# Kernel optimization log

Hardware: AMD Instinct MI355X
Metric: run time of the kernel (lower is better)

## Reference

```python
import jax, jax.numpy as jnp
import numpy as np

N_NODES = 100000
N_EDGES = 1000000
EMB = 64
HID = 64
N_CLASSES = 1
LEAKY_SLOPE = 0.01  # flax.linen.leaky_relu default


def setup_inputs() -> dict:
    key = jax.random.key(0)
    k1, k2, k3, k4, k5 = jax.random.split(key, 5)
    node_ids = jnp.arange(N_NODES, dtype=jnp.int32)
    senders = jax.random.randint(k1, (N_EDGES,), 0, N_NODES, dtype=jnp.int32)
    receivers = jax.random.randint(k2, (N_EDGES,), 0, N_NODES, dtype=jnp.int32)
    embed_table = jax.random.normal(k3, (N_NODES, EMB), dtype=jnp.float32) * 0.05
    W1 = jax.random.normal(k4, (EMB, HID), dtype=jnp.float32) * (1.0 / np.sqrt(EMB))
    W2 = jax.random.normal(k5, (HID, N_CLASSES), dtype=jnp.float32) * (1.0 / np.sqrt(HID))
    b2 = jnp.zeros((N_CLASSES,), dtype=jnp.float32)
    return {"node_ids": node_ids, "senders": senders, "receivers": receivers,
            "embed_table": embed_table, "W1": W1, "W2": W2, "b2": b2}


def gcn_aggregate(x, senders, receivers, n_nodes, symmetric):
    # Faithful to jraph.GraphConvolution: update_node_fn is applied BEFORE this.
    if symmetric:
        ones = jnp.ones_like(senders, dtype=x.dtype)
        send_deg = jax.ops.segment_sum(ones, senders, num_segments=n_nodes)
        recv_deg = jax.ops.segment_sum(ones, receivers, num_segments=n_nodes)
        x = x * jax.lax.rsqrt(jnp.maximum(send_deg, 1.0))[:, None]
        x = jax.ops.segment_sum(x[senders], receivers, num_segments=n_nodes)  # [N, d]
        x = x * jax.lax.rsqrt(jnp.maximum(recv_deg, 1.0))[:, None]
    else:
        x = jax.ops.segment_sum(x[senders], receivers, num_segments=n_nodes)
    return x


def reference(node_ids, senders, receivers, embed_table, W1, W2, b2):
    n = node_ids.shape[0]
    # GraphMapFeatures(embed_node_fn=nn.Embed(...))
    x = embed_table[node_ids]                      # [N, EMB]
    # GraphConvolution(Dense(hidden, use_bias=False), symmetric_normalization=True)
    x = x @ W1                                     # [N, HID]
    x = gcn_aggregate(x, senders, receivers, n, symmetric=True)
    x = jax.nn.leaky_relu(x, negative_slope=LEAKY_SLOPE)
    # GraphConvolution(Dense(classes), symmetric_normalization=False)
    x = x @ W2 + b2                                # [N, C]
    x = gcn_aggregate(x, senders, receivers, n, symmetric=False)
    return jax.nn.sigmoid(x)
```

## Files before the change

kernel.cpp:

```cpp
#include <hip/hip_runtime.h>
#include <hip/hip_bf16.h>

#define N_NODES 100000
#define N_EDGES 1000000
#define SCAN_B 256
#define N_BLOCKS_SCAN ((N_NODES + SCAN_B - 1) / SCAN_B)
#define H_BLOCKS 1024

#define CHUNKS 40
#define CHUNK_E 25000
#define HWORDS 25000


__device__ __forceinline__ unsigned f32_to_bf16(float v) {
    unsigned u = __float_as_uint(v);
    return (u + 0x7fffu + ((u >> 16) & 1u)) >> 16;
}

__global__ void k_hist8(const int4* __restrict__ s4,
                        const int4* __restrict__ r4,
                        unsigned* __restrict__ ghist_s8,
                        unsigned* __restrict__ ghist_r8,
                        unsigned char* __restrict__ rank8) {
    __shared__ unsigned lds[HWORDS];
    int b   = blockIdx.x;
    int isR = (b < CHUNKS);
    int c   = isR ? b : b - CHUNKS;
    int t   = threadIdx.x;

    for (int w = t; w < HWORDS; w += 1024) lds[w] = 0u;
    __syncthreads();

    int beg = c * (CHUNK_E / 4);
    int end = beg + CHUNK_E / 4;
    if (isR) {
        for (int q = beg + t; q < end; q += 1024) {
            int4 v = r4[q];
            int sh0 = (v.x & 3) * 8, sh1 = (v.y & 3) * 8;
            int sh2 = (v.z & 3) * 8, sh3 = (v.w & 3) * 8;
            unsigned o0 = atomicAdd(&lds[v.x >> 2], 1u << sh0);
            unsigned o1 = atomicAdd(&lds[v.y >> 2], 1u << sh1);
            unsigned o2 = atomicAdd(&lds[v.z >> 2], 1u << sh2);
            unsigned o3 = atomicAdd(&lds[v.w >> 2], 1u << sh3);
            uchar4 rk;
            rk.x = (unsigned char)((o0 >> sh0) & 0xffu);
            rk.y = (unsigned char)((o1 >> sh1) & 0xffu);
            rk.z = (unsigned char)((o2 >> sh2) & 0xffu);
            rk.w = (unsigned char)((o3 >> sh3) & 0xffu);
            *(uchar4*)(rank8 + 4 * (size_t)q) = rk;
        }
    } else {
        for (int q = beg + t; q < end; q += 1024) {
            int4 v = s4[q];
            atomicAdd(&lds[v.x >> 2], 1u << ((v.x & 3) * 8));
            atomicAdd(&lds[v.y >> 2], 1u << ((v.y & 3) * 8));
            atomicAdd(&lds[v.z >> 2], 1u << ((v.z & 3) * 8));
            atomicAdd(&lds[v.w >> 2], 1u << ((v.w & 3) * 8));
        }
    }
    __syncthreads();

    uint4* __restrict__ dst =
        (uint4*)((isR ? ghist_r8 : ghist_s8) + (size_t)c * HWORDS);
    const uint4* lsrc = (const uint4*)lds;
    for (int w = t; w < HWORDS / 4; w += 1024) dst[w] = lsrc[w];
}

__global__ void k_scanA(const unsigned char* __restrict__ gs8,
                        const unsigned char* __restrict__ gr8,
                        unsigned char* __restrict__ base8,
                        int* __restrict__ cnt_r,
                        float* __restrict__ rs,
                        int* __restrict__ blockSums) {
    __shared__ int s[SCAN_B];
    int t = threadIdx.x;
    int idx = blockIdx.x * SCAN_B + t;
    int v = 0;
    if (idx < N_NODES) {
        unsigned ss = 0;
#pragma unroll
        for (int c = 0; c < CHUNKS; ++c) ss += gs8[(size_t)c * N_NODES + idx];
        rs[idx] = rsqrtf(fmaxf((float)ss, 1.0f));
        unsigned run = 0;
#pragma unroll
        for (int c = 0; c < CHUNKS; ++c) {
            base8[(size_t)c * N_NODES + idx] = (unsigned char)run;
            run += gr8[(size_t)c * N_NODES + idx];
        }
        v = (int)run;
        cnt_r[idx] = v;
    }
    s[t] = v;
    __syncthreads();
    for (int off = 1; off < SCAN_B; off <<= 1) {
        int x = (t >= off) ? s[t - off] : 0;
        __syncthreads();
        s[t] += x;
        __syncthreads();
    }
    if (t == SCAN_B - 1) blockSums[blockIdx.x] = s[t];
}

__global__ void k_scanCD_h(const int* __restrict__ cnt_r,
                           const int* __restrict__ blockSums,
                           int* __restrict__ row_start,
                           const float* __restrict__ emb,
                           const float* __restrict__ rs,
                           const float* __restrict__ W1,
                           unsigned short* __restrict__ h16) {
    __shared__ int s[SCAN_B];
    int t = threadIdx.x;
    int b = blockIdx.x;

    if (b < N_BLOCKS_SCAN) {
        int acc = 0;
        for (int j = t; j < b; j += SCAN_B) acc += blockSums[j];
        s[t] = acc;
        __syncthreads();
        for (int off = SCAN_B / 2; off > 0; off >>= 1) {
            if (t < off) s[t] += s[t + off];
            __syncthreads();
        }
        int blockOff = s[0];
        __syncthreads();

        int idx = b * SCAN_B + t;
        int v = (idx < N_NODES) ? cnt_r[idx] : 0;
        s[t] = v;
        __syncthreads();
        for (int off = 1; off < SCAN_B; off <<= 1) {
            int x = (t >= off) ? s[t - off] : 0;
            __syncthreads();
            s[t] += x;
            __syncthreads();
        }
        if (idx < N_NODES) row_start[idx] = blockOff + s[t] - v;
        if (b == 0 && t == 0) row_start[N_NODES] = N_EDGES;
    } else {
        int lane = t & 63;
        int wib  = t >> 6;
        int gw   = (b - N_BLOCKS_SCAN) * 4 + wib;
        const int nw = H_BLOCKS * 4;

        float w1c[64];
#pragma unroll
        for (int k = 0; k < 64; ++k) w1c[k] = W1[k * 64 + lane];

        for (int n = gw; n < N_NODES; n += nw) {
            float e = emb[(size_t)n * 64 + lane] * rs[n];
            float a = 0.f;
            int ei = __float_as_int(e);
#pragma unroll
            for (int k = 0; k < 64; ++k)
                a += __int_as_float(__builtin_amdgcn_readlane(ei, k)) * w1c[k];
            h16[(size_t)n * 64 + lane] = (unsigned short)f32_to_bf16(a);
        }
    }
}

__global__ void k_fill(const int4* __restrict__ s4,
                       const int4* __restrict__ r4,
                       const uchar4* __restrict__ rk4,
                       const unsigned char* __restrict__ base8,
                       const int* __restrict__ row_start,
                       int* __restrict__ col) {
    int i = blockIdx.x * blockDim.x + threadIdx.x;
    if (i >= N_EDGES / 4) return;
    int c = (4 * i) / CHUNK_E;
    const unsigned char* __restrict__ bs = base8 + (size_t)c * N_NODES;
    int4 s = s4[i];
    int4 r = r4[i];
    uchar4 rk = rk4[i];
    col[row_start[r.x] + bs[r.x] + rk.x] = s.x;
    col[row_start[r.y] + bs[r.y] + rk.y] = s.y;
    col[row_start[r.z] + bs[r.z] + rk.z] = s.z;
    col[row_start[r.w] + bs[r.w] + rk.w] = s.w;
}

__global__ void k_agg_post(const int* __restrict__ row_start,
                           const int* __restrict__ col,
                           const unsigned* __restrict__ h32,
                           const float* __restrict__ W2,
                           const float* __restrict__ b2,
                           float* __restrict__ z) {
    int gtid = blockIdx.x * blockDim.x + threadIdx.x;
    int wid  = gtid >> 6;
    int lane = threadIdx.x & 63;
    int half = lane >> 5;
    int hl   = lane & 31;
    int n = wid * 2 + half;
    if (n >= N_NODES) return;

    int start = row_start[n];
    int end   = row_start[n + 1];
    float a0 = 0.f, a1 = 0.f;
    int i = start;
    for (; i + 3 < end; i += 4) {
        int s0 = col[i], s1 = col[i + 1], s2 = col[i + 2], s3 = col[i + 3];
        unsigned u0 = h32[(size_t)s0 * 32 + hl];
        unsigned u1 = h32[(size_t)s1 * 32 + hl];
        unsigned u2 = h32[(size_t)s2 * 32 + hl];
        unsigned u3 = h32[(size_t)s3 * 32 + hl];
        a0 += (__uint_as_float(u0 << 16) + __uint_as_float(u1 << 16)) +
              (__uint_as_float(u2 << 16) + __uint_as_float(u3 << 16));
        a1 += (__uint_as_float(u0 & 0xffff0000u) + __uint_as_float(u1 & 0xffff0000u)) +
              (__uint_as_float(u2 & 0xffff0000u) + __uint_as_float(u3 & 0xffff0000u));
    }
    for (; i < end; ++i) {
        unsigned u = h32[(size_t)col[i] * 32 + hl];
        a0 += __uint_as_float(u << 16);
        a1 += __uint_as_float(u & 0xffff0000u);
    }

    float rsq = rsqrtf(fmaxf((float)(end - start), 1.0f));
    float x0 = a0 * rsq, x1 = a1 * rsq;
    x0 = (x0 > 0.f) ? x0 : 0.01f * x0;
    x1 = (x1 > 0.f) ? x1 : 0.01f * x1;
    float2 w2 = ((const float2*)W2)[hl];
    float p = x0 * w2.x + x1 * w2.y;
#pragma unroll
    for (int off = 16; off > 0; off >>= 1) p += __shfl_xor(p, off, 64);
    if (hl == 0) z[n] = p + b2[0];
}

__global__ void k_agg2_sigmoid(const int* __restrict__ row_start,
                               const int* __restrict__ col,
                               const float* __restrict__ z,
                               float* __restrict__ out) {
    int n = blockIdx.x * blockDim.x + threadIdx.x;
    if (n >= N_NODES) return;
    int start = row_start[n];
    int end   = row_start[n + 1];
    float acc = 0.f;
    int i = start;
    for (; i + 3 < end; i += 4) {
        float a = z[col[i]],     b = z[col[i + 1]];
        float c = z[col[i + 2]], d = z[col[i + 3]];
        acc += (a + b) + (c + d);
    }
    for (; i < end; ++i) acc += z[col[i]];
    out[n] = 1.0f / (1.0f + expf(-acc));
}

extern "C" void kernel_launch(void* const* d_in, const int* in_sizes, int n_in,
                              void* d_out, int out_size, void* d_ws, size_t ws_size,
                              hipStream_t stream) {
    const int* senders    = (const int*)d_in[1];
    const int* receivers  = (const int*)d_in[2];
    const float* emb      = (const float*)d_in[3];
    const float* W1       = (const float*)d_in[4];
    const float* W2       = (const float*)d_in[5];
    const float* b2       = (const float*)d_in[6];
    float* out            = (float*)d_out;

    char* ws = (char*)d_ws;
    unsigned char*  ghist_s8  = (unsigned char*)(ws);
    unsigned char*  ghist_r8  = (unsigned char*)(ws + 4000000);
    unsigned char*  base8     = (unsigned char*)(ws + 8000000);
    unsigned char*  rank8     = (unsigned char*)(ws + 12000000);
    int*            cnt_r     = (int*)(ws + 13000000);
    int*            row_start = (int*)(ws + 13400000);
    int*            blockSums = (int*)(ws + 13800016);
    float*          rs        = (float*)(ws + 13801600);
    int*            col       = (int*)(ws + 14201600);
    unsigned short* h16       = (unsigned short*)(ws + 18201600);
    float*          z         = (float*)(ws + 31001600);

    const int B = 256;
    const int QBLK = (N_EDGES / 4 + B - 1) / B;

    k_hist8<<<2 * CHUNKS, 1024, 0, stream>>>(
        (const int4*)senders, (const int4*)receivers,
        (unsigned*)ghist_s8, (unsigned*)ghist_r8, rank8);
    k_scanA<<<N_BLOCKS_SCAN, SCAN_B, 0, stream>>>(
        ghist_s8, ghist_r8, base8, cnt_r, rs, blockSums);
    k_scanCD_h<<<N_BLOCKS_SCAN + H_BLOCKS, B, 0, stream>>>(
        cnt_r, blockSums, row_start, emb, rs, W1, h16);
    k_fill<<<QBLK, B, 0, stream>>>(
        (const int4*)senders, (const int4*)receivers,
        (const uchar4*)rank8, base8, row_start, col);
    k_agg_post<<<12500, B, 0, stream>>>(row_start, col, (const unsigned*)h16, W2, b2, z);
    k_agg2_sigmoid<<<(N_NODES + B - 1) / B, B, 0, stream>>>(row_start, col, z, out);
}
```

Before: 183.9 us.

## Split per-node scans and aggregations across multiple lanes with wave shuffles

The column scan now uses four lanes per node with shuffle prefix sums, and the block scan uses wave shuffles, so the row_start kernel only adds offsets. The W1 matvec gets four independent accumulators to break the dependency chain. Layer-1 aggregation gives each node a full wave: eight edge slots each load 16-byte bf16 vectors, followed by a shuffle reduction. The layer-2 aggregation spreads each node's edges over four lanes. The aim is more parallelism and memory-level concurrency on the gather-heavy stages, at the cost of extra shuffle work and more wave launches.

```diff
diff --git a/kernel.cpp b/kernel.cpp
--- a/kernel.cpp
+++ b/kernel.cpp
@@ -4,7 +4,8 @@
 #define N_NODES 100000
 #define N_EDGES 1000000
 #define SCAN_B 256
-#define N_BLOCKS_SCAN ((N_NODES + SCAN_B - 1) / SCAN_B)
+#define N_BLOCKS_RS ((N_NODES + 255) / 256)
+#define N_BLOCKS_A  ((N_NODES + 63) / 64)
 #define H_BLOCKS 1024
 
 #define CHUNKS 40
@@ -69,39 +70,59 @@
 __global__ void k_scanA(const unsigned char* __restrict__ gs8,
                         const unsigned char* __restrict__ gr8,
                         unsigned char* __restrict__ base8,
-                        int* __restrict__ cnt_r,
+                        int* __restrict__ part,
                         float* __restrict__ rs,
                         int* __restrict__ blockSums) {
-    __shared__ int s[SCAN_B];
+    __shared__ int s[64];
     int t = threadIdx.x;
-    int idx = blockIdx.x * SCAN_B + t;
-    int v = 0;
-    if (idx < N_NODES) {
+    int g = t >> 2, sl = t & 3;
+    int node = blockIdx.x * 64 + g;
+    int total = 0;
+    if (node < N_NODES) {
         unsigned ss = 0;
 #pragma unroll
-        for (int c = 0; c < CHUNKS; ++c) ss += gs8[(size_t)c * N_NODES + idx];
-        rs[idx] = rsqrtf(fmaxf((float)ss, 1.0f));
-        unsigned run = 0;
-#pragma unroll
-        for (int c = 0; c < CHUNKS; ++c) {
-            base8[(size_t)c * N_NODES + idx] = (unsigned char)run;
-            run += gr8[(size_t)c * N_NODES + idx];
-        }
-        v = (int)run;
-        cnt_r[idx] = v;
-    }
-    s[t] = v;
+        for (int k = 0; k < 10; ++k)
+            ss += gs8[(size_t)(sl * 10 + k) * N_NODES + node];
+        ss += __shfl_xor(ss, 1, 64);
+        ss += __shfl_xor(ss, 2, 64);
+        if (sl == 0) rs[node] = rsqrtf(fmaxf((float)ss, 1.0f));
+
+        unsigned rv[10];
+        unsigned rsum = 0;
+#pragma unroll
+        for (int k = 0; k < 10; ++k) {
+            rv[k] = gr8[(size_t)(sl * 10 + k) * N_NODES + node];
+            rsum += rv[k];
+        }
+        unsigned x = rsum;
+        unsigned u1 = __shfl_up(x, 1, 4); if (sl >= 1) x += u1;
+        unsigned u2 = __shfl_up(x, 2, 4); if (sl >= 2) x += u2;
+        unsigned run = x - rsum;
+        total = (int)__shfl(x, 3, 4);
+#pragma unroll
+        for (int k = 0; k < 10; ++k) {
+            base8[(size_t)(sl * 10 + k) * N_NODES + node] = (unsigned char)run;
+            run += rv[k];
+        }
+    }
+    if (sl == 0) s[g] = total;
     __syncthreads();
-    for (int off = 1; off < SCAN_B; off <<= 1) {
-        int x = (t >= off) ? s[t - off] : 0;
-        __syncthreads();
-        s[t] += x;
-        __syncthreads();
-    }
-    if (t == SCAN_B - 1) blockSums[blockIdx.x] = s[t];
-}
-
-__global__ void k_scanCD_h(const int* __restrict__ cnt_r,
+    if (t < 64) {
+        int v = s[t];
+        int acc = v;
+#pragma unroll
+        for (int off = 1; off < 64; off <<= 1) {
+            int y = __shfl_up(acc, off, 64);
+            if (t >= off) acc += y;
+        }
+        s[t] = acc - v;
+        if (t == 63) blockSums[blockIdx.x] = acc;
+    }
+    __syncthreads();
+    if (sl == 0 && node < N_NODES) part[node] = s[g];
+}
+
+__global__ void k_scanCD_h(const int* __restrict__ part,
                            const int* __restrict__ blockSums,
                            int* __restrict__ row_start,
                            const float* __restrict__ emb,
@@ -109,12 +130,13 @@
                            const float* __restrict__ W1,
                            unsigned short* __restrict__ h16) {
     __shared__ int s[SCAN_B];
+    __shared__ int gsum[4];
     int t = threadIdx.x;
     int b = blockIdx.x;
 
-    if (b < N_BLOCKS_SCAN) {
+    if (b < N_BLOCKS_RS) {
         int acc = 0;
-        for (int j = t; j < b; j += SCAN_B) acc += blockSums[j];
+        for (int j = t; j < 4 * b; j += SCAN_B) acc += blockSums[j];
         s[t] = acc;
         __syncthreads();
         for (int off = SCAN_B / 2; off > 0; off >>= 1) {
@@ -122,24 +144,22 @@
             __syncthreads();
         }
         int blockOff = s[0];
+        if (t < 4)
+            gsum[t] = (4 * b + t < N_BLOCKS_A) ? blockSums[4 * b + t] : 0;
         __syncthreads();
 
-        int idx = b * SCAN_B + t;
-        int v = (idx < N_NODES) ? cnt_r[idx] : 0;
-        s[t] = v;
-        __syncthreads();
-        for (int off = 1; off < SCAN_B; off <<= 1) {
-            int x = (t >= off) ? s[t - off] : 0;
-            __syncthreads();
-            s[t] += x;
-            __syncthreads();
-        }
-        if (idx < N_NODES) row_start[idx] = blockOff + s[t] - v;
+        int gi = t >> 6;
+        int goff = blockOff;
+        if (gi > 0) goff += gsum[0];
+        if (gi > 1) goff += gsum[1];
+        if (gi > 2) goff += gsum[2];
+        int n = b * SCAN_B + t;
+        if (n < N_NODES) row_start[n] = goff + part[n];
         if (b == 0 && t == 0) row_start[N_NODES] = N_EDGES;
     } else {
         int lane = t & 63;
         int wib  = t >> 6;
-        int gw   = (b - N_BLOCKS_SCAN) * 4 + wib;
+        int gw   = (b - N_BLOCKS_RS) * 4 + wib;
         const int nw = H_BLOCKS * 4;
 
         float w1c[64];
@@ -148,11 +168,16 @@
 
         for (int n = gw; n < N_NODES; n += nw) {
             float e = emb[(size_t)n * 64 + lane] * rs[n];
-            float a = 0.f;
+            float a0 = 0.f, a1 = 0.f, a2 = 0.f, a3 = 0.f;
             int ei = __float_as_int(e);
 #pragma unroll
-            for (int k = 0; k < 64; ++k)
-                a += __int_as_float(__builtin_amdgcn_readlane(ei, k)) * w1c[k];
+            for (int k = 0; k < 16; ++k) {
+                a0 += __int_as_float(__builtin_amdgcn_readlane(ei, 4 * k + 0)) * w1c[4 * k + 0];
+                a1 += __int_as_float(__builtin_amdgcn_readlane(ei, 4 * k + 1)) * w1c[4 * k + 1];
+                a2 += __int_as_float(__builtin_amdgcn_readlane(ei, 4 * k + 2)) * w1c[4 * k + 2];
+                a3 += __int_as_float(__builtin_amdgcn_readlane(ei, 4 * k + 3)) * w1c[4 * k + 3];
+            }
+            float a = (a0 + a1) + (a2 + a3);
             h16[(size_t)n * 64 + lane] = (unsigned short)f32_to_bf16(a);
         }
     }
@@ -179,67 +204,76 @@
 
 __global__ void k_agg_post(const int* __restrict__ row_start,
                            const int* __restrict__ col,
-                           const unsigned* __restrict__ h32,
+                           const uint4* __restrict__ h128,
                            const float* __restrict__ W2,
                            const float* __restrict__ b2,
                            float* __restrict__ z) {
-    int gtid = blockIdx.x * blockDim.x + threadIdx.x;
-    int wid  = gtid >> 6;
+    int wid  = (blockIdx.x * blockDim.x + threadIdx.x) >> 6;
     int lane = threadIdx.x & 63;
-    int half = lane >> 5;
-    int hl   = lane & 31;
-    int n = wid * 2 + half;
-    if (n >= N_NODES) return;
-
-    int start = row_start[n];
-    int end   = row_start[n + 1];
-    float a0 = 0.f, a1 = 0.f;
-    int i = start;
-    for (; i + 3 < end; i += 4) {
-        int s0 = col[i], s1 = col[i + 1], s2 = col[i + 2], s3 = col[i + 3];
-        unsigned u0 = h32[(size_t)s0 * 32 + hl];
-        unsigned u1 = h32[(size_t)s1 * 32 + hl];
-        unsigned u2 = h32[(size_t)s2 * 32 + hl];
-        unsigned u3 = h32[(size_t)s3 * 32 + hl];
-        a0 += (__uint_as_float(u0 << 16) + __uint_as_float(u1 << 16)) +
-              (__uint_as_float(u2 << 16) + __uint_as_float(u3 << 16));
-        a1 += (__uint_as_float(u0 & 0xffff0000u) + __uint_as_float(u1 & 0xffff0000u)) +
-              (__uint_as_float(u2 & 0xffff0000u) + __uint_as_float(u3 & 0xffff0000u));
-    }
-    for (; i < end; ++i) {
-        unsigned u = h32[(size_t)col[i] * 32 + hl];
-        a0 += __uint_as_float(u << 16);
-        a1 += __uint_as_float(u & 0xffff0000u);
-    }
-
+    if (wid >= N_NODES) return;
+    int eslot = lane >> 3;
+    int fq    = lane & 7;
+
+    int start = row_start[wid];
+    int end   = row_start[wid + 1];
+    float a0 = 0.f, a1 = 0.f, a2 = 0.f, a3 = 0.f;
+    float a4 = 0.f, a5 = 0.f, a6 = 0.f, a7 = 0.f;
+    for (int i = start + eslot; i < end; i += 8) {
+        int sx = col[i];
+        uint4 u = h128[(size_t)sx * 8 + fq];
+        a0 += __uint_as_float(u.x << 16);
+        a1 += __uint_as_float(u.x & 0xffff0000u);
+        a2 += __uint_as_float(u.y << 16);
+        a3 += __uint_as_float(u.y & 0xffff0000u);
+        a4 += __uint_as_float(u.z << 16);
+        a5 += __uint_as_float(u.z & 0xffff0000u);
+        a6 += __uint_as_float(u.w << 16);
+        a7 += __uint_as_float(u.w & 0xffff0000u);
+    }
+#pragma unroll
+    for (int off = 8; off < 64; off <<= 1) {
+        a0 += __shfl_xor(a0, off, 64);
+        a1 += __shfl_xor(a1, off, 64);
+        a2 += __shfl_xor(a2, off, 64);
+        a3 += __shfl_xor(a3, off, 64);
+        a4 += __shfl_xor(a4, off, 64);
+        a5 += __shfl_xor(a5, off, 64);
+        a6 += __shfl_xor(a6, off, 64);
+        a7 += __shfl_xor(a7, off, 64);
+    }
     float rsq = rsqrtf(fmaxf((float)(end - start), 1.0f));
-    float x0 = a0 * rsq, x1 = a1 * rsq;
-    x0 = (x0 > 0.f) ? x0 : 0.01f * x0;
-    x1 = (x1 > 0.f) ? x1 : 0.01f * x1;
-    float2 w2 = ((const float2*)W2)[hl];
-    float p = x0 * w2.x + x1 * w2.y;
-#pragma unroll
-    for (int off = 16; off > 0; off >>= 1) p += __shfl_xor(p, off, 64);
-    if (hl == 0) z[n] = p + b2[0];
+    float4 wA = ((const float4*)W2)[fq * 2];
+    float4 wB = ((const float4*)W2)[fq * 2 + 1];
+    float p = 0.f, x;
+    x = a0 * rsq; x = (x > 0.f) ? x : 0.01f * x; p += x * wA.x;
+    x = a1 * rsq; x = (x > 0.f) ? x : 0.01f * x; p += x * wA.y;
+    x = a2 * rsq; x = (x > 0.f) ? x : 0.01f * x; p += x * wA.z;
+    x = a3 * rsq; x = (x > 0.f) ? x : 0.01f * x; p += x * wA.w;
+    x = a4 * rsq; x = (x > 0.f) ? x : 0.01f * x; p += x * wB.x;
+    x = a5 * rsq; x = (x > 0.f) ? x : 0.01f * x; p += x * wB.y;
+    x = a6 * rsq; x = (x > 0.f) ? x : 0.01f * x; p += x * wB.z;
+    x = a7 * rsq; x = (x > 0.f) ? x : 0.01f * x; p += x * wB.w;
+    p += __shfl_xor(p, 1, 64);
+    p += __shfl_xor(p, 2, 64);
+    p += __shfl_xor(p, 4, 64);
+    if (lane == 0) z[wid] = p + b2[0];
 }
 
 __global__ void k_agg2_sigmoid(const int* __restrict__ row_start,
                                const int* __restrict__ col,
                                const float* __restrict__ z,
                                float* __restrict__ out) {
-    int n = blockIdx.x * blockDim.x + threadIdx.x;
+    int gtid = blockIdx.x * blockDim.x + threadIdx.x;
+    int n  = gtid >> 2;
+    int sl = gtid & 3;
     if (n >= N_NODES) return;
     int start = row_start[n];
     int end   = row_start[n + 1];
     float acc = 0.f;
-    int i = start;
-    for (; i + 3 < end; i += 4) {
-        float a = z[col[i]],     b = z[col[i + 1]];
-        float c = z[col[i + 2]], d = z[col[i + 3]];
-        acc += (a + b) + (c + d);
-    }
-    for (; i < end; ++i) acc += z[col[i]];
-    out[n] = 1.0f / (1.0f + expf(-acc));
+    for (int i = start + sl; i < end; i += 4) acc += z[col[i]];
+    acc += __shfl_xor(acc, 1, 64);
+    acc += __shfl_xor(acc, 2, 64);
+    if (sl == 0) out[n] = 1.0f / (1.0f + expf(-acc));
 }
 
 extern "C" void kernel_launch(void* const* d_in, const int* in_sizes, int n_in,
@@ -258,13 +292,13 @@
     unsigned char*  ghist_r8  = (unsigned char*)(ws + 4000000);
     unsigned char*  base8     = (unsigned char*)(ws + 8000000);
     unsigned char*  rank8     = (unsigned char*)(ws + 12000000);
-    int*            cnt_r     = (int*)(ws + 13000000);
+    int*            part      = (int*)(ws + 13000000);
     int*            row_start = (int*)(ws + 13400000);
     int*            blockSums = (int*)(ws + 13800016);
-    float*          rs        = (float*)(ws + 13801600);
-    int*            col       = (int*)(ws + 14201600);
-    unsigned short* h16       = (unsigned short*)(ws + 18201600);
-    float*          z         = (float*)(ws + 31001600);
+    float*          rs        = (float*)(ws + 13807600);
+    int*            col       = (int*)(ws + 14207600);
+    unsigned short* h16       = (unsigned short*)(ws + 18207616);
+    float*          z         = (float*)(ws + 31007616);
 
     const int B = 256;
     const int QBLK = (N_EDGES / 4 + B - 1) / B;
@@ -272,13 +306,15 @@
     k_hist8<<<2 * CHUNKS, 1024, 0, stream>>>(
         (const int4*)senders, (const int4*)receivers,
         (unsigned*)ghist_s8, (unsigned*)ghist_r8, rank8);
-    k_scanA<<<N_BLOCKS_SCAN, SCAN_B, 0, stream>>>(
-        ghist_s8, ghist_r8, base8, cnt_r, rs, blockSums);
-    k_scanCD_h<<<N_BLOCKS_SCAN + H_BLOCKS, B, 0, stream>>>(
-        cnt_r, blockSums, row_start, emb, rs, W1, h16);
+    k_scanA<<<N_BLOCKS_A, B, 0, stream>>>(
+        ghist_s8, ghist_r8, base8, part, rs, blockSums);
+    k_scanCD_h<<<N_BLOCKS_RS + H_BLOCKS, B, 0, stream>>>(
+        part, blockSums, row_start, emb, rs, W1, h16);
     k_fill<<<QBLK, B, 0, stream>>>(
         (const int4*)senders, (const int4*)receivers,
         (const uchar4*)rank8, base8, row_start, col);
-    k_agg_post<<<12500, B, 0, stream>>>(row_start, col, (const unsigned*)h16, W2, b2, z);
-    k_agg2_sigmoid<<<(N_NODES + B - 1) / B, B, 0, stream>>>(row_start, col, z, out);
-}
+    k_agg_post<<<(N_NODES * 64) / B, B, 0, stream>>>(
+        row_start, col, (const uint4*)h16, W2, b2, z);
+    k_agg2_sigmoid<<<(N_NODES * 4 + B - 1) / B, B, 0, stream>>>(
+        row_start, col, z, out);
+}
```

After: 184.3 us. No clear change (+0.2%).
